# Optimization experiments

Hardware: AMD Instinct MI355X
Metric: run time of the kernel (lower is better)

## Reference

```python
import jax, jax.numpy as jnp
import numpy as np

B, S, D = 2, 2048, 1024
E, K, F = 8, 2, 4 * 1024  # num_experts, top_k, fc_rate*embed_dim
T = B * S


def setup_inputs() -> dict:
    key = jax.random.key(0)
    ks = jax.random.split(key, 8)
    w = lambda k, shape: jax.random.normal(k, shape, jnp.float32) * 0.02
    return {
        "hidden_states": jax.random.normal(ks[0], (B, S, D), jnp.float32),
        "noise": jax.random.normal(ks[1], (T, E), jnp.float32),  # randn_like in router
        "Wg": w(ks[2], (D, E)), "bg": jnp.zeros((E,), jnp.float32),
        "Wn": w(ks[3], (D, E)), "bn": jnp.zeros((E,), jnp.float32),
        "W1": w(ks[4], (E, D, F)), "b1": jnp.zeros((E, F), jnp.float32),
        "W2": w(ks[5], (E, F, D)), "b2": jnp.zeros((E, D), jnp.float32),
    }


def reference(hidden_states, noise, Wg, bg, Wn, bn, W1, b1, W2, b2):
    b, s, d = hidden_states.shape
    x = hidden_states.reshape(-1, d)  # [T, D]

    # --- NoisyTopkRouter ---
    gate_logits = x @ Wg + bg                        # [T, E]
    noise_logits = x @ Wn + bn                       # [T, E]
    noisy_logits = gate_logits + noise * jax.nn.softplus(noise_logits)
    rw = jax.nn.softmax(noisy_logits.astype(jnp.float32), axis=-1)
    top_w, top_i = jax.lax.top_k(rw, K)              # [T, K]
    top_w = top_w / top_w.sum(-1, keepdims=True)
    top_w = top_w.astype(x.dtype)

    # Dense per-token combine coefficients: coef[t,e] = sum_k top_w[t,k]*[top_i[t,k]==e]
    tok = jnp.arange(x.shape[0])[:, None]
    coef = jnp.zeros((x.shape[0], E), x.dtype).at[tok, top_i].add(top_w)  # [T, E]

    # --- Experts: Linear -> GELU(exact) -> Linear (dropout = identity, eval mode) ---
    h = jax.nn.gelu(jnp.einsum('td,edf->tef', x, W1) + b1, approximate=False)  # [T,E,F]
    y = jnp.einsum('tef,efd->ted', h, W2) + b2                                  # [T,E,D]
    out = jnp.einsum('ted,te->td', y, coef)                                     # [T,D]

    return out.reshape(b, s, d), noisy_logits, gate_logits
```

## Files before the change

kernel.cpp:

```cpp
#include <hip/hip_runtime.h>
#include <hip/hip_bf16.h>

#define T_TOK 4096
#define D_DIM 1024
#define E_NUM 8
#define F_DIM 4096
#define NPAIR 8192

#define BM 128
#define BN 128
#define BK 64

typedef float f32x4 __attribute__((ext_vector_type(4)));
typedef __bf16 bf16x8 __attribute__((ext_vector_type(8)));
typedef unsigned short u16x8 __attribute__((ext_vector_type(8)));

__device__ __forceinline__ unsigned short f2bf(float f) {
    unsigned int u = __float_as_uint(f);
    u += 0x7fffu + ((u >> 16) & 1u);
    return (unsigned short)(u >> 16);
}

typedef const __attribute__((address_space(1))) void GV;
typedef __attribute__((address_space(3))) void LV;

__device__ __forceinline__ void load_lds16(const void* g, void* l) {
    __builtin_amdgcn_global_load_lds((GV*)g, (LV*)l, 16, 0, 0);
}

__device__ __forceinline__ bf16x8 lds_frag(const unsigned short* S, int row, int cs) {
    int byte = row * (BK * 2) + ((cs * 2) ^ ((row & 7) << 4));
    return *(const bf16x8*)((const char*)S + byte);
}

__global__ __launch_bounds__(256) void router_kernel(
    const float* __restrict__ x, const float* __restrict__ noise,
    const float* __restrict__ Wg, const float* __restrict__ bg,
    const float* __restrict__ Wn, const float* __restrict__ bn,
    float* __restrict__ out_noisy, float* __restrict__ out_gate,
    int* __restrict__ tk_idx, float* __restrict__ tk_w)
{
    int lane = threadIdx.x & 63;
    int t = blockIdx.x * 4 + (threadIdx.x >> 6);
    const float* xr = x + (size_t)t * D_DIM;

    float ag[E_NUM] = {}, an[E_NUM] = {};
    for (int it = 0; it < D_DIM / 64; ++it) {
        int d = it * 64 + lane;
        float xv = xr[d];
        float4 g0 = *(const float4*)(Wg + (size_t)d * E_NUM);
        float4 g1 = *(const float4*)(Wg + (size_t)d * E_NUM + 4);
        float4 m0 = *(const float4*)(Wn + (size_t)d * E_NUM);
        float4 m1 = *(const float4*)(Wn + (size_t)d * E_NUM + 4);
        ag[0] += xv * g0.x; ag[1] += xv * g0.y; ag[2] += xv * g0.z; ag[3] += xv * g0.w;
        ag[4] += xv * g1.x; ag[5] += xv * g1.y; ag[6] += xv * g1.z; ag[7] += xv * g1.w;
        an[0] += xv * m0.x; an[1] += xv * m0.y; an[2] += xv * m0.z; an[3] += xv * m0.w;
        an[4] += xv * m1.x; an[5] += xv * m1.y; an[6] += xv * m1.z; an[7] += xv * m1.w;
    }
    #pragma unroll
    for (int off = 32; off > 0; off >>= 1) {
        #pragma unroll
        for (int e = 0; e < E_NUM; ++e) {
            ag[e] += __shfl_xor(ag[e], off);
            an[e] += __shfl_xor(an[e], off);
        }
    }
    if (lane == 0) {
        float nz[E_NUM];
        #pragma unroll
        for (int e = 0; e < E_NUM; ++e) {
            float g = ag[e] + bg[e];
            float nn = an[e] + bn[e];
            float sp = fmaxf(nn, 0.f) + log1pf(expf(-fabsf(nn)));
            float z = g + noise[(size_t)t * E_NUM + e] * sp;
            out_gate[(size_t)t * E_NUM + e] = g;
            out_noisy[(size_t)t * E_NUM + e] = z;
            nz[e] = z;
        }
        int e0 = 0;
        #pragma unroll
        for (int e = 1; e < E_NUM; ++e) if (nz[e] > nz[e0]) e0 = e;
        int e1 = (e0 == 0) ? 1 : 0;
        #pragma unroll
        for (int e = 0; e < E_NUM; ++e) if (e != e0 && nz[e] > nz[e1]) e1 = e;
        float b = expf(nz[e1] - nz[e0]);
        float w0 = 1.f / (1.f + b);
        float w1 = b / (1.f + b);
        tk_idx[t * 2] = e0;  tk_idx[t * 2 + 1] = e1;
        tk_w[t * 2] = w0;    tk_w[t * 2 + 1] = w1;
    }
}

__global__ __launch_bounds__(256) void scan_scatter_kernel(
    const int* __restrict__ tk_idx,
    int* __restrict__ perm, int* __restrict__ meta)
{
    __shared__ int cnt[256][E_NUM];
    __shared__ int soff[E_NUM];
    int tid = threadIdx.x;
    const int PPT = NPAIR / 256;
    int p0 = tid * PPT;

    int c[E_NUM] = {};
    for (int i = 0; i < PPT; ++i) c[tk_idx[p0 + i]]++;
    #pragma unroll
    for (int e = 0; e < E_NUM; ++e) cnt[tid][e] = c[e];
    __syncthreads();

    if (tid < E_NUM) {
        int s = 0;
        for (int j = 0; j < 256; ++j) { int v = cnt[j][tid]; cnt[j][tid] = s; s += v; }
        soff[tid] = s;
    }
    __syncthreads();

    if (tid == 0) {
        int off = 0, nt = 0;
        for (int e = 0; e < E_NUM; ++e) {
            int ce = soff[e];
            meta[1 + e] = off;
            meta[9 + e] = ce;
            for (int j = 0; j < ce; j += BM) {
                meta[32 + nt]  = e;
                meta[160 + nt] = off + j;
                meta[288 + nt] = off + ce;
                nt++;
            }
            off += ce;
        }
        meta[0] = nt;
    }
    __syncthreads();
    if (tid < E_NUM) soff[tid] = meta[1 + tid];
    __syncthreads();

    int pos[E_NUM];
    #pragma unroll
    for (int e = 0; e < E_NUM; ++e) pos[e] = soff[e] + cnt[tid][e];
    for (int i = 0; i < PPT; ++i) {
        int e = tk_idx[p0 + i];
        perm[pos[e]++] = p0 + i;
    }
}

__global__ __launch_bounds__(256) void convert_x_kernel(
    const float* __restrict__ x, unsigned short* __restrict__ xb)
{
    size_t i = ((size_t)blockIdx.x * 256 + threadIdx.x) * 8;
    float4 a = *(const float4*)(x + i);
    float4 b = *(const float4*)(x + i + 4);
    u16x8 o;
    o[0] = f2bf(a.x); o[1] = f2bf(a.y); o[2] = f2bf(a.z); o[3] = f2bf(a.w);
    o[4] = f2bf(b.x); o[5] = f2bf(b.y); o[6] = f2bf(b.z); o[7] = f2bf(b.w);
    *(u16x8*)(xb + i) = o;
}

__global__ __launch_bounds__(256) void transpose_kernel(
    const float* __restrict__ W, unsigned short* __restrict__ WT, int R, int C)
{
    __shared__ float tile[32][33];
    int e = blockIdx.z;
    int c0 = blockIdx.x * 32, r0 = blockIdx.y * 32;
    int tx = threadIdx.x & 31, ty = threadIdx.x >> 5;
    const float* src = W + (size_t)e * R * C;
    #pragma unroll
    for (int i = 0; i < 4; ++i)
        tile[ty + 8 * i][tx] = src[(size_t)(r0 + ty + 8 * i) * C + c0 + tx];
    __syncthreads();
    unsigned short* dst = WT + (size_t)e * C * R;
    #pragma unroll
    for (int i = 0; i < 4; ++i)
        dst[(size_t)(c0 + ty + 8 * i) * R + r0 + tx] = f2bf(tile[tx][ty + 8 * i]);
}

__global__ __launch_bounds__(256, 4) void fc1_kernel(
    const unsigned short* __restrict__ xb,
    const unsigned short* __restrict__ W1T,
    const float* __restrict__ b1,
    const int* __restrict__ perm,
    const int* __restrict__ meta,
    unsigned short* __restrict__ h)
{
    const int nwg = 71 * (F_DIM / BN);
    const int cpx = nwg >> 3;
    int bid = blockIdx.x;
    int wg = (bid & 7) * cpx + (bid >> 3);
    int tile = wg >> 5;
    int n0 = (wg & 31) * BN;
    if (tile >= meta[0]) return;
    int e    = meta[32 + tile];
    int rs   = meta[160 + tile];
    int rend = meta[288 + tile];

    __shared__ __align__(16) unsigned short As[BM * BK];
    __shared__ __align__(16) unsigned short Bs[BN * BK];

    int tid = threadIdx.x, lane = tid & 63, wv = tid >> 6;
    int wm = (wv >> 1) * 64, wn = (wv & 1) * 64;
    int csw = ((tid & 7) ^ ((tid >> 3) & 7)) * 8;

    const unsigned short* asrc[4];
    #pragma unroll
    for (int i = 0; i < 4; ++i) {
        int q = tid + i * 256;
        int pos = rs + (q >> 3); if (pos >= NPAIR) pos = NPAIR - 1;
        int t = perm[pos] >> 1;
        asrc[i] = xb + (size_t)t * D_DIM + csw;
    }
    const unsigned short* bbase = W1T + ((size_t)e * F_DIM + n0 + wv * 32 + (lane >> 3)) * D_DIM + csw;

    f32x4 acc[4][4] = {};

    const int NT = D_DIM / BK;
    for (int t = 0; t < NT; ++t) {
        int k0 = t * BK;
        #pragma unroll
        for (int i = 0; i < 4; ++i)
            load_lds16(asrc[i] + k0, &As[(wv * 64 + i * 256) * 8]);
        #pragma unroll
        for (int j = 0; j < 4; ++j)
            load_lds16(bbase + (size_t)(j * 8) * D_DIM + k0, &Bs[(wv * 32 + j * 8) * BK]);
        asm volatile("s_waitcnt vmcnt(0)" ::: "memory");
        __builtin_amdgcn_s_barrier();
        #pragma unroll
        for (int kk = 0; kk < BK; kk += 32) {
            bf16x8 af[4], bf[4];
            #pragma unroll
            for (int m = 0; m < 4; ++m)
                af[m] = lds_frag(As, wm + m * 16 + (lane & 15), kk + (lane >> 4) * 8);
            #pragma unroll
            for (int n = 0; n < 4; ++n)
                bf[n] = lds_frag(Bs, wn + n * 16 + (lane & 15), kk + (lane >> 4) * 8);
            #pragma unroll
            for (int m = 0; m < 4; ++m)
                #pragma unroll
                for (int n = 0; n < 4; ++n)
                    acc[m][n] = __builtin_amdgcn_mfma_f32_16x16x32_bf16(af[m], bf[n], acc[m][n], 0, 0, 0);
        }
        asm volatile("s_waitcnt lgkmcnt(0)" ::: "memory");
        __builtin_amdgcn_s_barrier();
    }

    #pragma unroll
    for (int m = 0; m < 4; ++m) {
        #pragma unroll
        for (int j = 0; j < 4; ++j) {
            int r = wm + m * 16 + (lane >> 4) * 4 + j;
            int pos = rs + r;
            if (pos >= rend) continue;
            #pragma unroll
            for (int n = 0; n < 4; ++n) {
                int col = n0 + wn + n * 16 + (lane & 15);
                float v = acc[m][n][j] + b1[e * F_DIM + col];
                v = 0.5f * v * (1.f + erff(v * 0.70710678118654752f));
                h[(size_t)pos * F_DIM + col] = f2bf(v);
            }
        }
    }
}

__global__ __launch_bounds__(256, 4) void fc2_kernel(
    const unsigned short* __restrict__ h,
    const unsigned short* __restrict__ W2T,
    const float* __restrict__ b2,
    const int* __restrict__ perm,
    const float* __restrict__ tk_w,
    const int* __restrict__ meta,
    float* __restrict__ out)
{
    const int nwg = 71 * (D_DIM / BN) * 2;
    const int cpx = nwg >> 3;
    int bid = blockIdx.x;
    int wg = (bid & 7) * cpx + (bid >> 3);
    int tile = wg >> 4;
    int rem  = wg & 15;
    int n0 = (rem >> 1) * BN;
    int ks = rem & 1;
    if (tile >= meta[0]) return;
    int e    = meta[32 + tile];
    int rs   = meta[160 + tile];
    int rend = meta[288 + tile];
    int kbeg = ks * (F_DIM / 2);

    __shared__ __align__(16) unsigned short As[BM * BK];
    __shared__ __align__(16) unsigned short Bs[BN * BK];

    int tid = threadIdx.x, lane = tid & 63, wv = tid >> 6;
    int wm = (wv >> 1) * 64, wn = (wv & 1) * 64;
    int csw = ((tid & 7) ^ ((tid >> 3) & 7)) * 8;

    const unsigned short* asrc[4];
    #pragma unroll
    for (int i = 0; i < 4; ++i) {
        int q = tid + i * 256;
        int pos = rs + (q >> 3); if (pos >= NPAIR) pos = NPAIR - 1;
        asrc[i] = h + (size_t)pos * F_DIM + kbeg + csw;
    }
    const unsigned short* bbase = W2T + ((size_t)e * D_DIM + n0 + wv * 32 + (lane >> 3)) * F_DIM
                                + kbeg + csw;

    f32x4 acc[4][4] = {};

    const int NT = (F_DIM / 2) / BK;
    for (int t = 0; t < NT; ++t) {
        int k0 = t * BK;
        #pragma unroll
        for (int i = 0; i < 4; ++i)
            load_lds16(asrc[i] + k0, &As[(wv * 64 + i * 256) * 8]);
        #pragma unroll
        for (int j = 0; j < 4; ++j)
            load_lds16(bbase + (size_t)(j * 8) * F_DIM + k0, &Bs[(wv * 32 + j * 8) * BK]);
        asm volatile("s_waitcnt vmcnt(0)" ::: "memory");
        __builtin_amdgcn_s_barrier();
        #pragma unroll
        for (int kk = 0; kk < BK; kk += 32) {
            bf16x8 af[4], bf[4];
            #pragma unroll
            for (int m = 0; m < 4; ++m)
                af[m] = lds_frag(As, wm + m * 16 + (lane & 15), kk + (lane >> 4) * 8);
            #pragma unroll
            for (int n = 0; n < 4; ++n)
                bf[n] = lds_frag(Bs, wn + n * 16 + (lane & 15), kk + (lane >> 4) * 8);
            #pragma unroll
            for (int m = 0; m < 4; ++m)
                #pragma unroll
                for (int n = 0; n < 4; ++n)
                    acc[m][n] = __builtin_amdgcn_mfma_f32_16x16x32_bf16(af[m], bf[n], acc[m][n], 0, 0, 0);
        }
        asm volatile("s_waitcnt lgkmcnt(0)" ::: "memory");
        __builtin_amdgcn_s_barrier();
    }

    #pragma unroll
    for (int m = 0; m < 4; ++m) {
        #pragma unroll
        for (int j = 0; j < 4; ++j) {
            int r = wm + m * 16 + (lane >> 4) * 4 + j;
            int pos = rs + r;
            if (pos >= rend) continue;
            int pr = perm[pos];
            int t = pr >> 1;
            float w = tk_w[pr];
            #pragma unroll
            for (int n = 0; n < 4; ++n) {
                int col = n0 + wn + n * 16 + (lane & 15);
                float base = (ks == 0) ? b2[e * D_DIM + col] : 0.f;
                float v = (acc[m][n][j] + base) * w;
                atomicAdd(&out[(size_t)t * D_DIM + col], v);
            }
        }
    }
}

extern "C" void kernel_launch(void* const* d_in, const int* in_sizes, int n_in,
                              void* d_out, int out_size, void* d_ws, size_t ws_size,
                              hipStream_t stream)
{
    const float* x     = (const float*)d_in[0];
    const float* noise = (const float*)d_in[1];
    const float* Wg    = (const float*)d_in[2];
    const float* bg    = (const float*)d_in[3];
    const float* Wn    = (const float*)d_in[4];
    const float* bn    = (const float*)d_in[5];
    const float* W1    = (const float*)d_in[6];
    const float* b1    = (const float*)d_in[7];
    const float* W2    = (const float*)d_in[8];
    const float* b2    = (const float*)d_in[9];

    float* out       = (float*)d_out;
    float* out_noisy = out + (size_t)T_TOK * D_DIM;
    float* out_gate  = out_noisy + (size_t)T_TOK * E_NUM;

    char* ws = (char*)d_ws;
    int*   tk_idx = (int*)ws;
    float* tk_w   = (float*)(ws + 32768);
    int*   perm   = (int*)(ws + 65536);
    int*   meta   = (int*)(ws + 98304);
    size_t off = 131072;
    unsigned short* xb   = (unsigned short*)(ws + off); off += (size_t)T_TOK * D_DIM * 2;
    unsigned short* W1T  = (unsigned short*)(ws + off); off += (size_t)E_NUM * F_DIM * D_DIM * 2;
    unsigned short* W2T  = (unsigned short*)(ws + off); off += (size_t)E_NUM * D_DIM * F_DIM * 2;
    unsigned short* hbuf = (unsigned short*)(ws + off); off += (size_t)NPAIR * F_DIM * 2;

    hipMemsetAsync(d_out, 0, (size_t)out_size * sizeof(float), stream);

    router_kernel<<<T_TOK / 4, 256, 0, stream>>>(x, noise, Wg, bg, Wn, bn,
                                                 out_noisy, out_gate, tk_idx, tk_w);
    scan_scatter_kernel<<<1, 256, 0, stream>>>(tk_idx, perm, meta);
    convert_x_kernel<<<(T_TOK * D_DIM) / (256 * 8), 256, 0, stream>>>(x, xb);
    transpose_kernel<<<dim3(F_DIM / 32, D_DIM / 32, E_NUM), 256, 0, stream>>>(W1, W1T, D_DIM, F_DIM);
    transpose_kernel<<<dim3(D_DIM / 32, F_DIM / 32, E_NUM), 256, 0, stream>>>(W2, W2T, F_DIM, D_DIM);

    fc1_kernel<<<71 * (F_DIM / BN), 256, 0, stream>>>(xb, W1T, b1, perm, meta, hbuf);
    fc2_kernel<<<71 * (D_DIM / BN) * 2, 256, 0, stream>>>(hbuf, W2T, b2, perm, tk_w, meta, out);
}
```

Before: 478.3 us.

## Multi-stage LDS pipelining in expert GEMMs, fuse x conversion, widen transpose tiles

Both expert GEMM kernels move from a single LDS buffer with a full vmcnt(0) wait to a 4-deep ring of LDS buffers, prefetching three K-tiles ahead with graded vmcnt waits so global loads overlap MFMA work. Launch bounds drop to 1 block per SM because each block now uses 128KB of LDS. The bf16 conversion of x is folded into the router kernel, removing one launch and a second read of x. The weight transpose moves to 64x64 tiles with float4 loads and 16-byte bf16 stores. The cost is much lower occupancy in the GEMMs and more register and LDS pressure.

```diff
diff --git a/kernel.cpp b/kernel.cpp
--- a/kernel.cpp
+++ b/kernel.cpp
@@ -14,6 +14,7 @@
 typedef float f32x4 __attribute__((ext_vector_type(4)));
 typedef __bf16 bf16x8 __attribute__((ext_vector_type(8)));
 typedef unsigned short u16x8 __attribute__((ext_vector_type(8)));
+typedef unsigned short u16x4 __attribute__((ext_vector_type(4)));
 
 __device__ __forceinline__ unsigned short f2bf(float f) {
     unsigned int u = __float_as_uint(f);
@@ -33,16 +34,27 @@
     return *(const bf16x8*)((const char*)S + byte);
 }
 
-__global__ __launch_bounds__(256) void router_kernel(
+__global__ __launch_bounds__(256) void router_convert_kernel(
     const float* __restrict__ x, const float* __restrict__ noise,
     const float* __restrict__ Wg, const float* __restrict__ bg,
     const float* __restrict__ Wn, const float* __restrict__ bn,
     float* __restrict__ out_noisy, float* __restrict__ out_gate,
-    int* __restrict__ tk_idx, float* __restrict__ tk_w)
+    int* __restrict__ tk_idx, float* __restrict__ tk_w,
+    unsigned short* __restrict__ xb)
 {
     int lane = threadIdx.x & 63;
     int t = blockIdx.x * 4 + (threadIdx.x >> 6);
     const float* xr = x + (size_t)t * D_DIM;
+    unsigned short* xbr = xb + (size_t)t * D_DIM;
+
+    #pragma unroll
+    for (int r = 0; r < 4; ++r) {
+        int d = r * 256 + lane * 4;
+        float4 v = *(const float4*)(xr + d);
+        u16x4 o;
+        o[0] = f2bf(v.x); o[1] = f2bf(v.y); o[2] = f2bf(v.z); o[3] = f2bf(v.w);
+        *(u16x4*)(xbr + d) = o;
+    }
 
     float ag[E_NUM] = {}, an[E_NUM] = {};
     for (int it = 0; it < D_DIM / 64; ++it) {
@@ -143,37 +155,53 @@
     }
 }
 
-__global__ __launch_bounds__(256) void convert_x_kernel(
-    const float* __restrict__ x, unsigned short* __restrict__ xb)
-{
-    size_t i = ((size_t)blockIdx.x * 256 + threadIdx.x) * 8;
-    float4 a = *(const float4*)(x + i);
-    float4 b = *(const float4*)(x + i + 4);
-    u16x8 o;
-    o[0] = f2bf(a.x); o[1] = f2bf(a.y); o[2] = f2bf(a.z); o[3] = f2bf(a.w);
-    o[4] = f2bf(b.x); o[5] = f2bf(b.y); o[6] = f2bf(b.z); o[7] = f2bf(b.w);
-    *(u16x8*)(xb + i) = o;
-}
-
 __global__ __launch_bounds__(256) void transpose_kernel(
     const float* __restrict__ W, unsigned short* __restrict__ WT, int R, int C)
 {
-    __shared__ float tile[32][33];
+    __shared__ float tile[64][65];
     int e = blockIdx.z;
-    int c0 = blockIdx.x * 32, r0 = blockIdx.y * 32;
-    int tx = threadIdx.x & 31, ty = threadIdx.x >> 5;
+    int c0 = blockIdx.x * 64, r0 = blockIdx.y * 64;
+    int tx = threadIdx.x & 15, ty = threadIdx.x >> 4;
     const float* src = W + (size_t)e * R * C;
     #pragma unroll
-    for (int i = 0; i < 4; ++i)
-        tile[ty + 8 * i][tx] = src[(size_t)(r0 + ty + 8 * i) * C + c0 + tx];
+    for (int j = 0; j < 4; ++j) {
+        int r = ty + 16 * j;
+        float4 v = *(const float4*)(src + (size_t)(r0 + r) * C + c0 + tx * 4);
+        *(float4*)&tile[r][tx * 4] = v;
+    }
     __syncthreads();
     unsigned short* dst = WT + (size_t)e * C * R;
-    #pragma unroll
-    for (int i = 0; i < 4; ++i)
-        dst[(size_t)(c0 + ty + 8 * i) * R + r0 + tx] = f2bf(tile[tx][ty + 8 * i]);
-}
-
-__global__ __launch_bounds__(256, 4) void fc1_kernel(
+    int sx = threadIdx.x & 7, sy = threadIdx.x >> 3;
+    #pragma unroll
+    for (int j = 0; j < 2; ++j) {
+        int c = sy + 32 * j;
+        u16x8 o;
+        #pragma unroll
+        for (int k = 0; k < 8; ++k) o[k] = f2bf(tile[sx * 8 + k][c]);
+        *(u16x8*)(dst + (size_t)(c0 + c) * R + r0 + sx * 8) = o;
+    }
+}
+
+#define GEMM_COMPUTE(Abuf, Bbuf) do {                                                      \
+    _Pragma("unroll")                                                                      \
+    for (int kk = 0; kk < BK; kk += 32) {                                                  \
+        bf16x8 af[4], bf[4];                                                               \
+        _Pragma("unroll")                                                                  \
+        for (int m_ = 0; m_ < 4; ++m_)                                                     \
+            af[m_] = lds_frag((Abuf), wm + m_ * 16 + (lane & 15), kk + (lane >> 4) * 8);   \
+        _Pragma("unroll")                                                                  \
+        for (int n_ = 0; n_ < 4; ++n_)                                                     \
+            bf[n_] = lds_frag((Bbuf), wn + n_ * 16 + (lane & 15), kk + (lane >> 4) * 8);   \
+        _Pragma("unroll")                                                                  \
+        for (int m_ = 0; m_ < 4; ++m_)                                                     \
+            _Pragma("unroll")                                                              \
+            for (int n_ = 0; n_ < 4; ++n_)                                                 \
+                acc[m_][n_] = __builtin_amdgcn_mfma_f32_16x16x32_bf16(af[m_], bf[n_],      \
+                                                                      acc[m_][n_], 0, 0, 0); \
+    }                                                                                      \
+} while (0)
+
+__global__ __launch_bounds__(256, 1) void fc1_kernel(
     const unsigned short* __restrict__ xb,
     const unsigned short* __restrict__ W1T,
     const float* __restrict__ b1,
@@ -192,8 +220,8 @@
     int rs   = meta[160 + tile];
     int rend = meta[288 + tile];
 
-    __shared__ __align__(16) unsigned short As[BM * BK];
-    __shared__ __align__(16) unsigned short Bs[BN * BK];
+    __shared__ __align__(16) unsigned short As[4][BM * BK];
+    __shared__ __align__(16) unsigned short Bs[4][BN * BK];
 
     int tid = threadIdx.x, lane = tid & 63, wv = tid >> 6;
     int wm = (wv >> 1) * 64, wn = (wv & 1) * 64;
@@ -211,35 +239,35 @@
 
     f32x4 acc[4][4] = {};
 
+#define STAGE1(k0, b) do {                                                          \
+    _Pragma("unroll")                                                               \
+    for (int i_ = 0; i_ < 4; ++i_)                                                  \
+        load_lds16(asrc[i_] + (k0), &As[b][(wv * 64 + i_ * 256) * 8]);              \
+    _Pragma("unroll")                                                               \
+    for (int j_ = 0; j_ < 4; ++j_)                                                  \
+        load_lds16(bbase + (size_t)(j_ * 8) * D_DIM + (k0), &Bs[b][(wv * 32 + j_ * 8) * BK]); \
+} while (0)
+
     const int NT = D_DIM / BK;
+    STAGE1(0, 0); STAGE1(BK, 1); STAGE1(2 * BK, 2);
     for (int t = 0; t < NT; ++t) {
-        int k0 = t * BK;
-        #pragma unroll
-        for (int i = 0; i < 4; ++i)
-            load_lds16(asrc[i] + k0, &As[(wv * 64 + i * 256) * 8]);
-        #pragma unroll
-        for (int j = 0; j < 4; ++j)
-            load_lds16(bbase + (size_t)(j * 8) * D_DIM + k0, &Bs[(wv * 32 + j * 8) * BK]);
-        asm volatile("s_waitcnt vmcnt(0)" ::: "memory");
+        int cb = t & 3;
+        if (t + 3 < NT) {
+            STAGE1((t + 3) * BK, (t + 3) & 3);
+            asm volatile("s_waitcnt vmcnt(24)" ::: "memory");
+        } else if (t + 3 == NT) {
+            asm volatile("s_waitcnt vmcnt(16)" ::: "memory");
+        } else if (t + 2 == NT) {
+            asm volatile("s_waitcnt vmcnt(8)" ::: "memory");
+        } else {
+            asm volatile("s_waitcnt vmcnt(0)" ::: "memory");
+        }
         __builtin_amdgcn_s_barrier();
-        #pragma unroll
-        for (int kk = 0; kk < BK; kk += 32) {
-            bf16x8 af[4], bf[4];
-            #pragma unroll
-            for (int m = 0; m < 4; ++m)
-                af[m] = lds_frag(As, wm + m * 16 + (lane & 15), kk + (lane >> 4) * 8);
-            #pragma unroll
-            for (int n = 0; n < 4; ++n)
-                bf[n] = lds_frag(Bs, wn + n * 16 + (lane & 15), kk + (lane >> 4) * 8);
-            #pragma unroll
-            for (int m = 0; m < 4; ++m)
-                #pragma unroll
-                for (int n = 0; n < 4; ++n)
-                    acc[m][n] = __builtin_amdgcn_mfma_f32_16x16x32_bf16(af[m], bf[n], acc[m][n], 0, 0, 0);
-        }
+        GEMM_COMPUTE(As[cb], Bs[cb]);
         asm volatile("s_waitcnt lgkmcnt(0)" ::: "memory");
         __builtin_amdgcn_s_barrier();
     }
+#undef STAGE1
 
     #pragma unroll
     for (int m = 0; m < 4; ++m) {
@@ -259,7 +287,7 @@
     }
 }
 
-__global__ __launch_bounds__(256, 4) void fc2_kernel(
+__global__ __launch_bounds__(256, 1) void fc2_kernel(
     const unsigned short* __restrict__ h,
     const unsigned short* __restrict__ W2T,
     const float* __restrict__ b2,
@@ -282,8 +310,8 @@
     int rend = meta[288 + tile];
     int kbeg = ks * (F_DIM / 2);
 
-    __shared__ __align__(16) unsigned short As[BM * BK];
-    __shared__ __align__(16) unsigned short Bs[BN * BK];
+    __shared__ __align__(16) unsigned short As[4][BM * BK];
+    __shared__ __align__(16) unsigned short Bs[4][BN * BK];
 
     int tid = threadIdx.x, lane = tid & 63, wv = tid >> 6;
     int wm = (wv >> 1) * 64, wn = (wv & 1) * 64;
@@ -301,35 +329,35 @@
 
     f32x4 acc[4][4] = {};
 
+#define STAGE2(k0, b) do {                                                          \
+    _Pragma("unroll")                                                               \
+    for (int i_ = 0; i_ < 4; ++i_)                                                  \
+        load_lds16(asrc[i_] + (k0), &As[b][(wv * 64 + i_ * 256) * 8]);              \
+    _Pragma("unroll")                                                               \
+    for (int j_ = 0; j_ < 4; ++j_)                                                  \
+        load_lds16(bbase + (size_t)(j_ * 8) * F_DIM + (k0), &Bs[b][(wv * 32 + j_ * 8) * BK]); \
+} while (0)
+
     const int NT = (F_DIM / 2) / BK;
+    STAGE2(0, 0); STAGE2(BK, 1); STAGE2(2 * BK, 2);
     for (int t = 0; t < NT; ++t) {
-        int k0 = t * BK;
-        #pragma unroll
-        for (int i = 0; i < 4; ++i)
-            load_lds16(asrc[i] + k0, &As[(wv * 64 + i * 256) * 8]);
-        #pragma unroll
-        for (int j = 0; j < 4; ++j)
-            load_lds16(bbase + (size_t)(j * 8) * F_DIM + k0, &Bs[(wv * 32 + j * 8) * BK]);
-        asm volatile("s_waitcnt vmcnt(0)" ::: "memory");
+        int cb = t & 3;
+        if (t + 3 < NT) {
+            STAGE2((t + 3) * BK, (t + 3) & 3);
+            asm volatile("s_waitcnt vmcnt(24)" ::: "memory");
+        } else if (t + 3 == NT) {
+            asm volatile("s_waitcnt vmcnt(16)" ::: "memory");
+        } else if (t + 2 == NT) {
+            asm volatile("s_waitcnt vmcnt(8)" ::: "memory");
+        } else {
+            asm volatile("s_waitcnt vmcnt(0)" ::: "memory");
+        }
         __builtin_amdgcn_s_barrier();
-        #pragma unroll
-        for (int kk = 0; kk < BK; kk += 32) {
-            bf16x8 af[4], bf[4];
-            #pragma unroll
-            for (int m = 0; m < 4; ++m)
-                af[m] = lds_frag(As, wm + m * 16 + (lane & 15), kk + (lane >> 4) * 8);
-            #pragma unroll
-            for (int n = 0; n < 4; ++n)
-                bf[n] = lds_frag(Bs, wn + n * 16 + (lane & 15), kk + (lane >> 4) * 8);
-            #pragma unroll
-            for (int m = 0; m < 4; ++m)
-                #pragma unroll
-                for (int n = 0; n < 4; ++n)
-                    acc[m][n] = __builtin_amdgcn_mfma_f32_16x16x32_bf16(af[m], bf[n], acc[m][n], 0, 0, 0);
-        }
+        GEMM_COMPUTE(As[cb], Bs[cb]);
         asm volatile("s_waitcnt lgkmcnt(0)" ::: "memory");
         __builtin_amdgcn_s_barrier();
     }
+#undef STAGE2
 
     #pragma unroll
     for (int m = 0; m < 4; ++m) {
@@ -384,12 +412,11 @@
 
     hipMemsetAsync(d_out, 0, (size_t)out_size * sizeof(float), stream);
 
-    router_kernel<<<T_TOK / 4, 256, 0, stream>>>(x, noise, Wg, bg, Wn, bn,
-                                                 out_noisy, out_gate, tk_idx, tk_w);
+    router_convert_kernel<<<T_TOK / 4, 256, 0, stream>>>(x, noise, Wg, bg, Wn, bn,
+                                                         out_noisy, out_gate, tk_idx, tk_w, xb);
     scan_scatter_kernel<<<1, 256, 0, stream>>>(tk_idx, perm, meta);
-    convert_x_kernel<<<(T_TOK * D_DIM) / (256 * 8), 256, 0, stream>>>(x, xb);
-    transpose_kernel<<<dim3(F_DIM / 32, D_DIM / 32, E_NUM), 256, 0, stream>>>(W1, W1T, D_DIM, F_DIM);
-    transpose_kernel<<<dim3(D_DIM / 32, F_DIM / 32, E_NUM), 256, 0, stream>>>(W2, W2T, F_DIM, D_DIM);
+    transpose_kernel<<<dim3(D_DIM / 64, F_DIM / 64, E_NUM), 256, 0, stream>>>(W2, W2T, F_DIM, D_DIM);
+    transpose_kernel<<<dim3(F_DIM / 64, D_DIM / 64, E_NUM), 256, 0, stream>>>(W1, W1T, D_DIM, F_DIM);
 
     fc1_kernel<<<71 * (F_DIM / BN), 256, 0, stream>>>(xb, W1T, b1, perm, meta, hbuf);
     fc2_kernel<<<71 * (D_DIM / BN) * 2, 256, 0, stream>>>(hbuf, W2T, b2, perm, tk_w, meta, out);
```

After: 733.1 us. +53.3%, slower.
